# Optimization experiments

Measured on AMD Instinct MI355X. Metric: run time of the kernel, lower is better.

Reference implementation:

```python
import jax, jax.numpy as jnp
import numpy as np

V = 8192
E = 262144
IN_DIM = 128
OUT_DIM = 128
NEG_SLOPE = 0.2


def setup_inputs() -> dict:
    key = jax.random.key(0)
    k1, k2, k3, k4 = jax.random.split(key, 4)
    h = jax.random.normal(k1, (V, IN_DIM), dtype=jnp.float32)
    edge_index = jax.random.randint(k2, (2, E), 0, V, dtype=jnp.int64)
    # nn.Linear weights: W (out_dim, in_dim), att (1, 2*out_dim), both bias-free
    W = jax.random.normal(k3, (OUT_DIM, IN_DIM), dtype=jnp.float32) / np.sqrt(IN_DIM)
    att_w = jax.random.normal(k4, (1, 2 * OUT_DIM), dtype=jnp.float32) / np.sqrt(2 * OUT_DIM)
    return {"h": h, "edge_index": edge_index, "W": W, "att_w": att_w}


def reference(h, edge_index, W, att_w):
    # h: (V, in_dim) -> (V, out_dim)
    hw = h @ W.T
    src, dst = edge_index[0], edge_index[1]
    # edge features: concat of endpoint embeddings -> (E, 2*out_dim)
    e = jnp.concatenate([hw[src], hw[dst]], axis=-1)
    # attention logits per edge, LeakyReLU(0.2)
    a = jax.nn.leaky_relu(jnp.squeeze(e @ att_w.T, -1), negative_slope=NEG_SLOPE)
    v = hw.shape[0]
    # faithful to original: dense V x V matrix, zeros on non-edges,
    # softmax over ALL columns (non-edges included as score 0)
    alpha = jnp.zeros((v, v), dtype=hw.dtype).at[src, dst].set(a)
    alpha = jax.nn.softmax(alpha, axis=-1)
    # dropout is identity in eval mode (deterministic reference)
    return alpha @ hw
```

## Files before the change

### kernel.cpp

```cpp
#include <hip/hip_runtime.h>
#include <hip/hip_bf16.h>
#include <math.h>


#define V 8192
#define E 262144
#define D 128
#define NEG_SLOPE 0.2f
#define CAP 96

__global__ __launch_bounds__(256) void k_hw(const float* __restrict__ h,
                                            const float* __restrict__ W,
                                            const float* __restrict__ att,
                                            float* __restrict__ hw,
                                            float* __restrict__ s1,
                                            float* __restrict__ s2,
                                            float* __restrict__ S) {
    __shared__ float Wt[D * 132];
    __shared__ float hs[8][D];
    __shared__ float atts[2 * D];
    for (int e = threadIdx.x; e < D * D; e += 256) {
        int o = e >> 7, k = e & 127;
        Wt[k * 132 + o] = W[e];
    }
    atts[threadIdx.x] = att[threadIdx.x];
    int c4 = (threadIdx.x & 31) * 4;
    int rsel = threadIdx.x >> 5;
    int rowbase = blockIdx.x * 32;
    float4 cs = make_float4(0.f, 0.f, 0.f, 0.f);
    for (int it = 0; it < 4; ++it) {
        int r0 = rowbase + it * 8;
        __syncthreads();
        for (int e = threadIdx.x; e < 8 * D; e += 256)
            hs[e >> 7][e & 127] = h[(r0 + (e >> 7)) * D + (e & 127)];
        __syncthreads();
        float a0 = 0.f, a1 = 0.f, a2 = 0.f, a3 = 0.f;
        const float* hrow = hs[rsel];
        #pragma unroll 8
        for (int k = 0; k < D; ++k) {
            float hk = hrow[k];
            float4 wv = *(const float4*)&Wt[k * 132 + c4];
            a0 += hk * wv.x; a1 += hk * wv.y; a2 += hk * wv.z; a3 += hk * wv.w;
        }
        int row = r0 + rsel;
        *(float4*)&hw[row * D + c4] = make_float4(a0, a1, a2, a3);
        cs.x += a0; cs.y += a1; cs.z += a2; cs.w += a3;
        float p1 = a0 * atts[c4] + a1 * atts[c4 + 1] + a2 * atts[c4 + 2] + a3 * atts[c4 + 3];
        float p2 = a0 * atts[D + c4] + a1 * atts[D + c4 + 1] + a2 * atts[D + c4 + 2] + a3 * atts[D + c4 + 3];
        #pragma unroll
        for (int m = 16; m; m >>= 1) {
            p1 += __shfl_xor(p1, m);
            p2 += __shfl_xor(p2, m);
        }
        if ((threadIdx.x & 31) == 0) { s1[row] = p1; s2[row] = p2; }
    }
    __syncthreads();
    hs[rsel][c4] = cs.x; hs[rsel][c4 + 1] = cs.y; hs[rsel][c4 + 2] = cs.z; hs[rsel][c4 + 3] = cs.w;
    __syncthreads();
    if (threadIdx.x < D) {
        float t = 0.f;
        #pragma unroll
        for (int r = 0; r < 8; ++r) t += hs[r][threadIdx.x];
        atomicAdd(&S[threadIdx.x], t);
    }
}

__global__ __launch_bounds__(256) void k_scatter(const int* __restrict__ ei,
                                                 const float* __restrict__ s1,
                                                 const float* __restrict__ s2,
                                                 int* __restrict__ cnt,
                                                 int2* __restrict__ bucket) {
    int e = blockIdx.x * 256 + threadIdx.x;
    int src = ei[e];
    int dst = ei[E + e];
    float a = s1[src] + s2[dst];
    a = a > 0.f ? a : NEG_SLOPE * a;
    float w = expf(a) - 1.f;
    int pos = atomicAdd(&cnt[src], 1);
    if (pos < CAP)
        bucket[src * CAP + pos] = make_int2(dst, __float_as_int(w));
}

__global__ __launch_bounds__(256) void k_row(const int2* __restrict__ bucket,
                                             const int* __restrict__ cnt,
                                             const float* __restrict__ hw,
                                             const float* __restrict__ S,
                                             float* __restrict__ out) {
    int row = (blockIdx.x * 256 + threadIdx.x) >> 6;
    int lane = threadIdx.x & 63;
    int deg = cnt[row];
    if (deg > CAP) deg = CAP;
    const int2* b = bucket + row * CAP;
    int2 e0 = b[lane];
    int2 e1 = (lane < CAP - 64) ? b[64 + lane] : make_int2(-1, 0);
    int d0 = e0.x; float w0 = __int_as_float(e0.y);
    int d1 = e1.x; float w1 = __int_as_float(e1.y);
    if (lane >= deg)      { d0 = -1; w0 = 0.f; }
    if (64 + lane >= deg) { d1 = -1; w1 = 0.f; }
    float2 acc = make_float2(0.f, 0.f);
    float dex = 0.f;
    int dmax0 = deg < 64 ? deg : 64;
    for (int j = 0; j < dmax0; ++j) {
        int   dj = __shfl(d0, j);
        float wj = __shfl(w0, j);
        bool dup = (d0 == dj) && (lane < j);
        if (__any(dup)) continue;
        float2 hv = *(const float2*)&hw[dj * D + lane * 2];
        acc.x += wj * hv.x; acc.y += wj * hv.y;
        dex += wj;
    }
    for (int j = 64; j < deg; ++j) {
        int   dj = __shfl(d1, j - 64);
        float wj = __shfl(w1, j - 64);
        bool dup = (d0 == dj) || ((d1 == dj) && (64 + lane < j));
        if (__any(dup)) continue;
        float2 hv = *(const float2*)&hw[dj * D + lane * 2];
        acc.x += wj * hv.x; acc.y += wj * hv.y;
        dex += wj;
    }
    float inv = 1.f / ((float)V + dex);
    float2 s = *(const float2*)&S[lane * 2];
    float2 o;
    o.x = (s.x + acc.x) * inv;
    o.y = (s.y + acc.y) * inv;
    *(float2*)&out[row * D + lane * 2] = o;
}

extern "C" void kernel_launch(void* const* d_in, const int* in_sizes, int n_in,
                              void* d_out, int out_size, void* d_ws, size_t ws_size,
                              hipStream_t stream) {
    const float* h   = (const float*)d_in[0];
    const int*   ei  = (const int*)d_in[1];
    const float* W   = (const float*)d_in[2];
    const float* att = (const float*)d_in[3];
    float* out = (float*)d_out;

    char* ws = (char*)d_ws;
    float* hw  = (float*)(ws);
    float* s1  = (float*)(ws + 4194304);
    float* s2  = (float*)(ws + 4227072);
    float* S   = (float*)(ws + 4259840);
    int*   cnt = (int*)(ws + 4260352);
    int2*  bucket = (int2*)(ws + 4293120);

    hipMemsetAsync(ws + 4259840, 0, 512 + 32768, stream);

    k_hw     <<<256,  256, 0, stream>>>(h, W, att, hw, s1, s2, S);
    k_scatter<<<1024, 256, 0, stream>>>(ei, s1, s2, cnt, bucket);
    k_row    <<<2048, 256, 0, stream>>>(bucket, cnt, hw, S, out);
}
```

Baseline: 117.8 us.

## Fold attention into input space and overlap edge scatter with the hw GEMM

Computes the attention scores s1/s2 directly from h using the precomputed vectors W^T·att, and the column sum S as W·(sum of h). This removes the dependency of the scatter on the hw matmul, so scatter blocks and GEMM blocks run concurrently in one merged launch. The memset is replaced by zeroing cnt inside the first kernel. k_row stages the bucket in LDS and masks duplicates with ballots instead of branching with __any. The cost is extra kernel complexity and a different floating-point summation order.

```diff
diff --git a/kernel.cpp b/kernel.cpp
--- a/kernel.cpp
+++ b/kernel.cpp
@@ -9,76 +9,135 @@
 #define NEG_SLOPE 0.2f
 #define CAP 96
 
-__global__ __launch_bounds__(256) void k_hw(const float* __restrict__ h,
-                                            const float* __restrict__ W,
-                                            const float* __restrict__ att,
-                                            float* __restrict__ hw,
-                                            float* __restrict__ s1,
-                                            float* __restrict__ s2,
-                                            float* __restrict__ S) {
-    __shared__ float Wt[D * 132];
-    __shared__ float hs[8][D];
+__global__ __launch_bounds__(256) void k_pre(const float* __restrict__ h,
+                                             const float* __restrict__ W,
+                                             const float* __restrict__ att,
+                                             float* __restrict__ Wt,
+                                             float* __restrict__ s1,
+                                             float* __restrict__ s2,
+                                             float* __restrict__ Pc,
+                                             int* __restrict__ cnt) {
     __shared__ float atts[2 * D];
-    for (int e = threadIdx.x; e < D * D; e += 256) {
-        int o = e >> 7, k = e & 127;
-        Wt[k * 132 + o] = W[e];
-    }
-    atts[threadIdx.x] = att[threadIdx.x];
-    int c4 = (threadIdx.x & 31) * 4;
-    int rsel = threadIdx.x >> 5;
-    int rowbase = blockIdx.x * 32;
-    float4 cs = make_float4(0.f, 0.f, 0.f, 0.f);
-    for (int it = 0; it < 4; ++it) {
-        int r0 = rowbase + it * 8;
+    __shared__ float us[2 * D];
+    __shared__ float csc[4][D];
+    int t = threadIdx.x, b = blockIdx.x;
+    atts[t] = att[t];
+    if (t < 32) cnt[b * 32 + t] = 0;
+    if (b < 64) {
+        int g = b * 256 + t;
+        Wt[(g & 127) * D + (g >> 7)] = W[g];
+    }
+    __syncthreads();
+    if (t < D) {
+        float u1 = 0.f, u2 = 0.f;
+        #pragma unroll 4
+        for (int o = 0; o < D; ++o) {
+            float wv = W[o * D + t];
+            u1 += wv * atts[o];
+            u2 += wv * atts[D + o];
+        }
+        us[t] = u1; us[D + t] = u2;
+    }
+    __syncthreads();
+    int wv = t >> 6, lane = t & 63;
+    float2 u1v = *(const float2*)&us[lane * 2];
+    float2 u2v = *(const float2*)&us[D + lane * 2];
+    int r0 = b * 32 + wv * 8;
+    float cx = 0.f, cy = 0.f;
+    for (int r = 0; r < 8; ++r) {
+        float2 hv = *(const float2*)&h[(r0 + r) * D + lane * 2];
+        cx += hv.x; cy += hv.y;
+        float p1 = hv.x * u1v.x + hv.y * u1v.y;
+        float p2 = hv.x * u2v.x + hv.y * u2v.y;
+        #pragma unroll
+        for (int m = 32; m; m >>= 1) { p1 += __shfl_xor(p1, m); p2 += __shfl_xor(p2, m); }
+        if (lane == 0) { s1[r0 + r] = p1; s2[r0 + r] = p2; }
+    }
+    *(float2*)&csc[wv][lane * 2] = make_float2(cx, cy);
+    __syncthreads();
+    if (t < D)
+        Pc[b * D + t] = csc[0][t] + csc[1][t] + csc[2][t] + csc[3][t];
+}
+
+__global__ __launch_bounds__(256) void k_mid(const float* __restrict__ h,
+                                             const float* __restrict__ Wt,
+                                             const float* __restrict__ W,
+                                             const int* __restrict__ ei,
+                                             const float* __restrict__ s1,
+                                             const float* __restrict__ s2,
+                                             const float* __restrict__ Pc,
+                                             float* __restrict__ hw,
+                                             float* __restrict__ S,
+                                             int* __restrict__ cnt,
+                                             int2* __restrict__ bucket) {
+    __shared__ float scr[4 * 16 * D];
+    int b = blockIdx.x, t = threadIdx.x;
+    if (b < 1024) {
+        int g = b * 256 + t;
+        int src = ei[g];
+        int dst = ei[E + g];
+        float a = s1[src] + s2[dst];
+        a = a > 0.f ? a : NEG_SLOPE * a;
+        float w = expf(a) - 1.f;
+        int pos = atomicAdd(&cnt[src], 1);
+        if (pos < CAP)
+            bucket[src * CAP + pos] = make_int2(dst, __float_as_int(w));
+    } else if (b == 1024) {
+        if (t < D) {
+            float c = 0.f;
+            #pragma unroll 4
+            for (int bb = 0; bb < 256; ++bb) c += Pc[bb * D + t];
+            scr[t] = c;
+        }
         __syncthreads();
-        for (int e = threadIdx.x; e < 8 * D; e += 256)
-            hs[e >> 7][e & 127] = h[(r0 + (e >> 7)) * D + (e & 127)];
+        if (t < D) {
+            float acc = 0.f;
+            #pragma unroll
+            for (int k = 0; k < D; k += 4) {
+                float4 wv = *(const float4*)&W[t * D + k];
+                float4 cv = *(const float4*)&scr[k];
+                acc += wv.x * cv.x + wv.y * cv.y + wv.z * cv.z + wv.w * cv.w;
+            }
+            S[t] = acc;
+        }
+    } else {
+        int r0 = (b - 1025) * 16;
+        int wv = t >> 6, lane = t & 63;
+        int c2 = lane * 2, ks = wv * 32;
+        float2 acc[16];
+        #pragma unroll
+        for (int r = 0; r < 16; ++r) acc[r] = make_float2(0.f, 0.f);
+        for (int kc = 0; kc < 32; kc += 4) {
+            int k = ks + kc;
+            float2 w0 = *(const float2*)&Wt[(k + 0) * D + c2];
+            float2 w1 = *(const float2*)&Wt[(k + 1) * D + c2];
+            float2 w2 = *(const float2*)&Wt[(k + 2) * D + c2];
+            float2 w3 = *(const float2*)&Wt[(k + 3) * D + c2];
+            #pragma unroll
+            for (int r = 0; r < 16; ++r) {
+                float4 hv = *(const float4*)&h[(r0 + r) * D + k];
+                acc[r].x += hv.x * w0.x + hv.y * w1.x + hv.z * w2.x + hv.w * w3.x;
+                acc[r].y += hv.x * w0.y + hv.y * w1.y + hv.z * w2.y + hv.w * w3.y;
+            }
+        }
+        #pragma unroll
+        for (int r = 0; r < 16; ++r)
+            *(float2*)&scr[(wv * 16 + r) * D + c2] = acc[r];
         __syncthreads();
-        float a0 = 0.f, a1 = 0.f, a2 = 0.f, a3 = 0.f;
-        const float* hrow = hs[rsel];
-        #pragma unroll 8
-        for (int k = 0; k < D; ++k) {
-            float hk = hrow[k];
-            float4 wv = *(const float4*)&Wt[k * 132 + c4];
-            a0 += hk * wv.x; a1 += hk * wv.y; a2 += hk * wv.z; a3 += hk * wv.w;
-        }
-        int row = r0 + rsel;
-        *(float4*)&hw[row * D + c4] = make_float4(a0, a1, a2, a3);
-        cs.x += a0; cs.y += a1; cs.z += a2; cs.w += a3;
-        float p1 = a0 * atts[c4] + a1 * atts[c4 + 1] + a2 * atts[c4 + 2] + a3 * atts[c4 + 3];
-        float p2 = a0 * atts[D + c4] + a1 * atts[D + c4 + 1] + a2 * atts[D + c4 + 2] + a3 * atts[D + c4 + 3];
-        #pragma unroll
-        for (int m = 16; m; m >>= 1) {
-            p1 += __shfl_xor(p1, m);
-            p2 += __shfl_xor(p2, m);
-        }
-        if ((threadIdx.x & 31) == 0) { s1[row] = p1; s2[row] = p2; }
-    }
-    __syncthreads();
-    hs[rsel][c4] = cs.x; hs[rsel][c4 + 1] = cs.y; hs[rsel][c4 + 2] = cs.z; hs[rsel][c4 + 3] = cs.w;
-    __syncthreads();
-    if (threadIdx.x < D) {
-        float t = 0.f;
-        #pragma unroll
-        for (int r = 0; r < 8; ++r) t += hs[r][threadIdx.x];
-        atomicAdd(&S[threadIdx.x], t);
-    }
-}
-
-__global__ __launch_bounds__(256) void k_scatter(const int* __restrict__ ei,
-                                                 const float* __restrict__ s1,
-                                                 const float* __restrict__ s2,
-                                                 int* __restrict__ cnt,
-                                                 int2* __restrict__ bucket) {
-    int e = blockIdx.x * 256 + threadIdx.x;
-    int src = ei[e];
-    int dst = ei[E + e];
-    float a = s1[src] + s2[dst];
-    a = a > 0.f ? a : NEG_SLOPE * a;
-    float w = expf(a) - 1.f;
-    int pos = atomicAdd(&cnt[src], 1);
-    if (pos < CAP)
-        bucket[src * CAP + pos] = make_int2(dst, __float_as_int(w));
+        int rq = t >> 4, c8 = (t & 15) * 8;
+        float4 v0 = make_float4(0.f, 0.f, 0.f, 0.f);
+        float4 v1 = make_float4(0.f, 0.f, 0.f, 0.f);
+        #pragma unroll
+        for (int w = 0; w < 4; ++w) {
+            const float* p = &scr[(w * 16 + rq) * D + c8];
+            float4 x = *(const float4*)p;
+            float4 y = *(const float4*)(p + 4);
+            v0.x += x.x; v0.y += x.y; v0.z += x.z; v0.w += x.w;
+            v1.x += y.x; v1.y += y.y; v1.z += y.z; v1.w += y.w;
+        }
+        *(float4*)&hw[(r0 + rq) * D + c8] = v0;
+        *(float4*)&hw[(r0 + rq) * D + c8 + 4] = v1;
+    }
 }
 
 __global__ __launch_bounds__(256) void k_row(const int2* __restrict__ bucket,
@@ -86,34 +145,42 @@
                                              const float* __restrict__ hw,
                                              const float* __restrict__ S,
                                              float* __restrict__ out) {
-    int row = (blockIdx.x * 256 + threadIdx.x) >> 6;
-    int lane = threadIdx.x & 63;
+    __shared__ int2 lb[4][CAP];
+    int t = threadIdx.x;
+    int wv = t >> 6, lane = t & 63;
+    int row = blockIdx.x * 4 + wv;
     int deg = cnt[row];
     if (deg > CAP) deg = CAP;
-    const int2* b = bucket + row * CAP;
-    int2 e0 = b[lane];
-    int2 e1 = (lane < CAP - 64) ? b[64 + lane] : make_int2(-1, 0);
-    int d0 = e0.x; float w0 = __int_as_float(e0.y);
-    int d1 = e1.x; float w1 = __int_as_float(e1.y);
-    if (lane >= deg)      { d0 = -1; w0 = 0.f; }
-    if (64 + lane >= deg) { d1 = -1; w1 = 0.f; }
+    const int2* bk = bucket + row * CAP;
+    int2 e0 = bk[lane];
+    int2 e1 = (lane < CAP - 64) ? bk[64 + lane] : make_int2(-1, 0);
+    int   d0 = (lane < deg)      ? e0.x : -1;
+    float w0 = (lane < deg)      ? __int_as_float(e0.y) : 0.f;
+    int   d1 = (64 + lane < deg) ? e1.x : -1;
+    float w1 = (64 + lane < deg) ? __int_as_float(e1.y) : 0.f;
+    lb[wv][lane] = make_int2(d0, __float_as_int(w0));
+    if (lane < CAP - 64) lb[wv][64 + lane] = make_int2(d1, __float_as_int(w1));
+    int n0 = deg < 64 ? deg : 64;
     float2 acc = make_float2(0.f, 0.f);
     float dex = 0.f;
-    int dmax0 = deg < 64 ? deg : 64;
-    for (int j = 0; j < dmax0; ++j) {
-        int   dj = __shfl(d0, j);
-        float wj = __shfl(w0, j);
-        bool dup = (d0 == dj) && (lane < j);
-        if (__any(dup)) continue;
+    const int2* myb = lb[wv];
+    for (int j = 0; j < n0; ++j) {
+        int2 ew = myb[j];
+        int dj = ew.x;
+        float wj = __int_as_float(ew.y);
+        unsigned long long m = __ballot(d0 == dj);
+        if (m & ((1ull << j) - 1ull)) wj = 0.f;
         float2 hv = *(const float2*)&hw[dj * D + lane * 2];
         acc.x += wj * hv.x; acc.y += wj * hv.y;
         dex += wj;
     }
     for (int j = 64; j < deg; ++j) {
-        int   dj = __shfl(d1, j - 64);
-        float wj = __shfl(w1, j - 64);
-        bool dup = (d0 == dj) || ((d1 == dj) && (64 + lane < j));
-        if (__any(dup)) continue;
+        int2 ew = myb[j];
+        int dj = ew.x;
+        float wj = __int_as_float(ew.y);
+        unsigned long long m0 = __ballot(d0 == dj);
+        unsigned long long m1 = __ballot(d1 == dj) & ((1ull << (j - 64)) - 1ull);
+        if (m0 | m1) wj = 0.f;
         float2 hv = *(const float2*)&hw[dj * D + lane * 2];
         acc.x += wj * hv.x; acc.y += wj * hv.y;
         dex += wj;
@@ -142,10 +209,10 @@
     float* S   = (float*)(ws + 4259840);
     int*   cnt = (int*)(ws + 4260352);
     int2*  bucket = (int2*)(ws + 4293120);
-
-    hipMemsetAsync(ws + 4259840, 0, 512 + 32768, stream);
-
-    k_hw     <<<256,  256, 0, stream>>>(h, W, att, hw, s1, s2, S);
-    k_scatter<<<1024, 256, 0, stream>>>(ei, s1, s2, cnt, bucket);
-    k_row    <<<2048, 256, 0, stream>>>(bucket, cnt, hw, S, out);
-}
+    float* Wt  = (float*)(ws + 10584576);
+    float* Pc  = (float*)(ws + 10650112);
+
+    k_pre<<<256,  256, 0, stream>>>(h, W, att, Wt, s1, s2, Pc, cnt);
+    k_mid<<<1537, 256, 0, stream>>>(h, Wt, W, ei, s1, s2, Pc, hw, S, cnt, bucket);
+    k_row<<<2048, 256, 0, stream>>>(bucket, cnt, hw, S, out);
+}
```

Result: slower. 130.7 us (+11.0%).
